# Kernel tuning notes

Measured on AMD Instinct MI355X. Metric: run time of the kernel, lower is better.

Reference implementation:

```python
import jax, jax.numpy as jnp
import numpy as np

DIM = 1024
HEADS = 16
DIM_HEAD = 64
INNER = HEADS * DIM_HEAD
SCALE = DIM_HEAD ** -0.5
LN_EPS = 1e-5
MASK_VALUE = -np.finfo(np.float32).max


def setup_inputs() -> dict:
    key = jax.random.key(0)
    ks = jax.random.split(key, 3)
    x = jax.random.normal(ks[0], (2, 2048, DIM), dtype=jnp.float32)
    w_qkv = jax.random.normal(ks[1], (DIM, 3 * INNER), dtype=jnp.float32) * (DIM ** -0.5)
    w_out = jax.random.normal(ks[2], (INNER, DIM), dtype=jnp.float32) * (INNER ** -0.5)
    ln_gamma = jnp.ones((DIM,), dtype=jnp.float32)
    ln_beta = jnp.zeros((DIM,), dtype=jnp.float32)
    return {"x": x, "ln_gamma": ln_gamma, "ln_beta": ln_beta, "w_qkv": w_qkv, "w_out": w_out}


def reference(x, ln_gamma, ln_beta, w_qkv, w_out):
    b, n, _ = x.shape
    # LayerNorm
    mu = jnp.mean(x, axis=-1, keepdims=True)
    var = jnp.mean(jnp.square(x - mu), axis=-1, keepdims=True)
    xn = (x - mu) * jax.lax.rsqrt(var + LN_EPS) * ln_gamma + ln_beta
    # QKV projection, split into heads: b n (h d) -> b h n d
    qkv = xn @ w_qkv  # [b, n, 3*inner]
    q, k, v = jnp.split(qkv, 3, axis=-1)
    def to_heads(t):
        return t.reshape(b, n, HEADS, DIM_HEAD).transpose(0, 2, 1, 3)
    q, k, v = to_heads(q), to_heads(k), to_heads(v)
    # scaled scores with diagonal excluded
    dots = jnp.einsum('bhnd,bhmd->bhnm', q, k) * SCALE
    eye = jnp.eye(n, dtype=bool)
    dots = jnp.where(eye, MASK_VALUE, dots)
    attn = jax.nn.softmax(dots, axis=-1)
    out = jnp.einsum('bhnm,bhmd->bhnd', attn, v)
    out = out.transpose(0, 2, 1, 3).reshape(b, n, INNER)
    return out @ w_out
```

## Files before the change

kernel.cpp:

```cpp
#include <hip/hip_runtime.h>


#define DIMM   1024
#define NSEQ   2048
#define BATCH  2
#define HEADS  16
#define DHEAD  64
#define QKVN   3072
#define MROWS  4096

typedef float          f32x4  __attribute__((ext_vector_type(4)));
typedef __bf16         bf16x8 __attribute__((ext_vector_type(8)));
typedef __bf16         bf16x4 __attribute__((ext_vector_type(4)));
typedef unsigned short u16x8  __attribute__((ext_vector_type(8)));
typedef unsigned short u16x4  __attribute__((ext_vector_type(4)));

#define QSCALE (0.125f * 1.4426950408889634f)

#if __has_builtin(__builtin_amdgcn_exp2f)
#define EXP2(x) __builtin_amdgcn_exp2f(x)
#else
#define EXP2(x) exp2f(x)
#endif

__device__ __forceinline__ unsigned short f2bf(float f) {
  unsigned u = __builtin_bit_cast(unsigned, f);
  u += 0x7FFFu + ((u >> 16) & 1u);
  return (unsigned short)(u >> 16);
}
__device__ __forceinline__ bf16x8 as_bf(u16x8 v) { return __builtin_bit_cast(bf16x8, v); }

__device__ __forceinline__ u16x4 cvt4(f32x4 v) {
  bf16x4 b;
  b[0] = (__bf16)v[0]; b[1] = (__bf16)v[1]; b[2] = (__bf16)v[2]; b[3] = (__bf16)v[3];
  return __builtin_bit_cast(u16x4, b);
}

__device__ __forceinline__ void gl_lds16(const unsigned short* g, unsigned short* l) {
  __builtin_amdgcn_global_load_lds(
      (const __attribute__((address_space(1))) unsigned*)g,
      (__attribute__((address_space(3))) unsigned*)l, 16, 0, 0);
}

__device__ __forceinline__ bf16x8 lds_frag(const unsigned short* base, int row, int chunk) {
  return as_bf(*(const u16x8*)&base[row * 64 + ((chunk ^ (row & 7)) << 3)]);
}

__device__ __forceinline__ bf16x8 lds_frag128(const unsigned short* base, int row, int chunk) {
  return as_bf(*(const u16x8*)&base[row * 128 + ((chunk ^ (row & 15)) << 3)]);
}

__device__ __forceinline__ void transpose_tile(
    const float* __restrict__ src, unsigned short* __restrict__ dst,
    int R, int C, int bx, int by, int tid) {
  __shared__ float t[32][33];
  const int rb = by * 32, cb = bx * 32;
  const int r0 = tid >> 5;
  const int c  = tid & 31;
#pragma unroll
  for (int i = 0; i < 4; ++i)
    t[r0 + i * 8][c] = src[(rb + r0 + i * 8) * C + cb + c];
  __syncthreads();
#pragma unroll
  for (int i = 0; i < 4; ++i)
    dst[(cb + r0 + i * 8) * R + rb + c] = f2bf(t[c][r0 + i * 8]);
}

__global__ __launch_bounds__(256) void prep_kernel(
    const float* __restrict__ x, const float* __restrict__ g,
    const float* __restrict__ be, const float* __restrict__ w_qkv,
    const float* __restrict__ w_out, unsigned short* __restrict__ xn,
    unsigned short* __restrict__ wqkvT, unsigned short* __restrict__ woutT) {
  const int bid = blockIdx.x, tid = threadIdx.x;
  if (bid < MROWS) {
    const int row = bid;
    const int wave = tid >> 6, lane = tid & 63;
    const float4 v = *(const float4*)&x[row * DIMM + tid * 4];
    float s  = v.x + v.y + v.z + v.w;
    float s2 = v.x * v.x + v.y * v.y + v.z * v.z + v.w * v.w;
#pragma unroll
    for (int o = 32; o >= 1; o >>= 1) { s += __shfl_xor(s, o); s2 += __shfl_xor(s2, o); }
    __shared__ float ps[4], ps2[4];
    if (lane == 0) { ps[wave] = s; ps2[wave] = s2; }
    __syncthreads();
    s  = ps[0] + ps[1] + ps[2] + ps[3];
    s2 = ps2[0] + ps2[1] + ps2[2] + ps2[3];
    const float mu  = s * (1.0f / DIMM);
    const float var = s2 * (1.0f / DIMM) - mu * mu;
    const float rs  = rsqrtf(var + 1e-5f);
    const float4 gg = *(const float4*)&g[tid * 4];
    const float4 bb = *(const float4*)&be[tid * 4];
    u16x4 o;
    o[0] = f2bf((v.x - mu) * rs * gg.x + bb.x);
    o[1] = f2bf((v.y - mu) * rs * gg.y + bb.y);
    o[2] = f2bf((v.z - mu) * rs * gg.z + bb.z);
    o[3] = f2bf((v.w - mu) * rs * gg.w + bb.w);
    *(u16x4*)&xn[row * DIMM + tid * 4] = o;
  } else {
    const int t = bid - MROWS;
    const int bx = t & 127, by = t >> 7;
    if (bx < QKVN / 32) transpose_tile(w_qkv, wqkvT, DIMM, QKVN, bx, by, tid);
    else                transpose_tile(w_out, woutT, DIMM, DIMM, bx - QKVN / 32, by, tid);
  }
}

__global__ __launch_bounds__(256, 3) void gemm_qkv_kernel(
    const unsigned short* __restrict__ A, const unsigned short* __restrict__ Bt,
    unsigned short* __restrict__ qb, unsigned short* __restrict__ kb,
    unsigned short* __restrict__ vtb) {
  __shared__ __attribute__((aligned(16))) unsigned short As[128 * 64];
  __shared__ __attribute__((aligned(16))) unsigned short Bs[128 * 64];
  const int tid = threadIdx.x;
  const int bm = blockIdx.y, bn = blockIdx.x;
  const int lane = tid & 63, wave = tid >> 6;
  const int l15 = lane & 15, quad = lane >> 4;
  const int wm = wave >> 1, wn = wave & 1;
  const int lrow = lane >> 3;
  const int gcol = ((lane & 7) ^ lrow) << 3;
  const unsigned short* Ab = A  + (bm * 128 + wave * 32 + lrow) * DIMM + gcol;
  const unsigned short* Bb = Bt + (bn * 128 + wave * 32 + lrow) * DIMM + gcol;
  const bool swap = (bn < 16);
  f32x4 acc[4][4] = {};

  for (int k0 = 0; k0 < DIMM; k0 += 64) {
#pragma unroll
    for (int j = 0; j < 4; ++j) {
      gl_lds16(Ab + j * 8 * DIMM + k0, &As[(wave * 32 + j * 8) * 64]);
      gl_lds16(Bb + j * 8 * DIMM + k0, &Bs[(wave * 32 + j * 8) * 64]);
    }
    __syncthreads();
#pragma unroll
    for (int kk = 0; kk < 2; ++kk) {
      bf16x8 af[4], bfr[4];
#pragma unroll
      for (int mi = 0; mi < 4; ++mi) af[mi]  = lds_frag(As, wm * 64 + mi * 16 + l15, kk * 4 + quad);
#pragma unroll
      for (int ni = 0; ni < 4; ++ni) bfr[ni] = lds_frag(Bs, wn * 64 + ni * 16 + l15, kk * 4 + quad);
      if (swap) {
#pragma unroll
        for (int mi = 0; mi < 4; ++mi)
#pragma unroll
          for (int ni = 0; ni < 4; ++ni)
            acc[mi][ni] = __builtin_amdgcn_mfma_f32_16x16x32_bf16(bfr[ni], af[mi], acc[mi][ni], 0, 0, 0);
      } else {
#pragma unroll
        for (int mi = 0; mi < 4; ++mi)
#pragma unroll
          for (int ni = 0; ni < 4; ++ni)
            acc[mi][ni] = __builtin_amdgcn_mfma_f32_16x16x32_bf16(af[mi], bfr[ni], acc[mi][ni], 0, 0, 0);
      }
    }
    __syncthreads();
  }

  if (swap) {
    const int colbase = bn * 128 + wn * 64;
    const int which = colbase >> 10;
    unsigned short* dst = which ? kb : qb;
    const float sc = which ? 1.0f : QSCALE;
#pragma unroll
    for (int mi = 0; mi < 4; ++mi) {
      const int m = bm * 128 + wm * 64 + mi * 16 + l15;
      const int bh0 = (m >> 11) * HEADS;
      const int n = m & 2047;
#pragma unroll
      for (int ni = 0; ni < 4; ++ni) {
        const int wc = (colbase & 1023) + ni * 16 + quad * 4;
        const int h = wc >> 6, dd = wc & 63;
        f32x4 v = acc[mi][ni] * sc;
        *(u16x4*)&dst[((bh0 + h) * NSEQ + n) * DHEAD + dd] = cvt4(v);
      }
    }
  } else {
    const int colbase = bn * 128 + wn * 64 - 2048;
#pragma unroll
    for (int mi = 0; mi < 4; ++mi) {
      const int m0 = bm * 128 + wm * 64 + mi * 16 + quad * 4;
      const int bh0 = (m0 >> 11) * HEADS;
      const int n0 = m0 & 2047;
#pragma unroll
      for (int ni = 0; ni < 4; ++ni) {
        const int vcol = colbase + ni * 16 + l15;
        const int h = vcol >> 6, dd = vcol & 63;
        *(u16x4*)&vtb[((bh0 + h) * DHEAD + dd) * NSEQ + n0] = cvt4(acc[mi][ni]);
      }
    }
  }
}

__global__ __launch_bounds__(256, 2) void attn_kernel(
    const unsigned short* __restrict__ qb, const unsigned short* __restrict__ kb,
    const unsigned short* __restrict__ vtb, unsigned short* __restrict__ attn_out) {
  __shared__ __attribute__((aligned(16))) unsigned short Ks[2][64 * 64];
  __shared__ __attribute__((aligned(16))) unsigned short Vts[2][64 * 64];
  __shared__ __attribute__((aligned(16))) unsigned short Ps[4][2][16][72];
  const int tid = threadIdx.x, wave = tid >> 6, lane = tid & 63;
  const int l15 = lane & 15, quad = lane >> 4;
  const int bh = blockIdx.x, qt = blockIdx.y;
  const int b = bh >> 4, h = bh & 15;
  const int qbase = qt * 128 + wave * 32;

  bf16x8 aq[2][2];
#pragma unroll
  for (int sub = 0; sub < 2; ++sub) {
    const unsigned short* qrow = qb + (bh * NSEQ + qbase + sub * 16 + l15) * DHEAD;
    aq[sub][0] = as_bf(*(const u16x8*)(qrow + quad * 8));
    aq[sub][1] = as_bf(*(const u16x8*)(qrow + 32 + quad * 8));
  }

  float lsum[2] = {0.f, 0.f};
  f32x4 occ[2][4] = {};

  const int lrow = lane >> 3;
  const int gcol = ((lane & 7) ^ lrow) << 3;
  const unsigned short* Kb = kb  + (bh * NSEQ + wave * 16 + lrow) * DHEAD + gcol;
  const unsigned short* Vb = vtb + (bh * DHEAD + wave * 16 + lrow) * NSEQ + gcol;

  gl_lds16(Kb,             &Ks[0][(wave * 16) * 64]);
  gl_lds16(Kb + 8 * DHEAD, &Ks[0][(wave * 16 + 8) * 64]);
  gl_lds16(Vb,             &Vts[0][(wave * 16) * 64]);
  gl_lds16(Vb + 8 * NSEQ,  &Vts[0][(wave * 16 + 8) * 64]);

  const int diag_it = qt * 2 + (wave >> 1);

  for (int it = 0; it < NSEQ / 64; ++it) {
    const int cur = it & 1;
    __syncthreads();
    if (it < NSEQ / 64 - 1) {
      const unsigned short* Kn = Kb + (it + 1) * 64 * DHEAD;
      const unsigned short* Vn = Vb + (it + 1) * 64;
      gl_lds16(Kn,             &Ks[cur ^ 1][(wave * 16) * 64]);
      gl_lds16(Kn + 8 * DHEAD, &Ks[cur ^ 1][(wave * 16 + 8) * 64]);
      gl_lds16(Vn,             &Vts[cur ^ 1][(wave * 16) * 64]);
      gl_lds16(Vn + 8 * NSEQ,  &Vts[cur ^ 1][(wave * 16 + 8) * 64]);
    }
    bf16x8 ak[2][4], av[2][4];
#pragma unroll
    for (int kk = 0; kk < 2; ++kk)
#pragma unroll
      for (int ct = 0; ct < 4; ++ct) {
        ak[kk][ct] = lds_frag(&Ks[cur][0],  ct * 16 + l15, kk * 4 + quad);
        av[kk][ct] = lds_frag(&Vts[cur][0], ct * 16 + l15, kk * 4 + quad);
      }

    f32x4 scc[2][4];
#pragma unroll
    for (int sub = 0; sub < 2; ++sub)
#pragma unroll
      for (int ct = 0; ct < 4; ++ct) scc[sub][ct] = (f32x4){-32.f, -32.f, -32.f, -32.f};
    __builtin_amdgcn_s_setprio(1);
#pragma unroll
    for (int sub = 0; sub < 2; ++sub)
#pragma unroll
      for (int kk = 0; kk < 2; ++kk)
#pragma unroll
        for (int ct = 0; ct < 4; ++ct)
          scc[sub][ct] = __builtin_amdgcn_mfma_f32_16x16x32_bf16(ak[kk][ct], aq[sub][kk], scc[sub][ct], 0, 0, 0);
    __builtin_amdgcn_s_setprio(0);

#pragma unroll
    for (int sub = 0; sub < 2; ++sub)
#pragma unroll
      for (int ct = 0; ct < 4; ++ct)
#pragma unroll
        for (int r = 0; r < 4; ++r) scc[sub][ct][r] = EXP2(scc[sub][ct][r]);

    if (it == diag_it) {
#pragma unroll
      for (int sub = 0; sub < 2; ++sub) {
        const int kvo_want = (wave & 1) * 32 + sub * 16 + l15;
#pragma unroll
        for (int ct = 0; ct < 4; ++ct)
#pragma unroll
          for (int r = 0; r < 4; ++r)
            if (ct * 16 + quad * 4 + r == kvo_want) scc[sub][ct][r] = 0.f;
      }
    }

#pragma unroll
    for (int sub = 0; sub < 2; ++sub) {
      f32x4 ps4 = (scc[sub][0] + scc[sub][1]) + (scc[sub][2] + scc[sub][3]);
      lsum[sub] += (ps4[0] + ps4[1]) + (ps4[2] + ps4[3]);
    }

#pragma unroll
    for (int sub = 0; sub < 2; ++sub)
#pragma unroll
      for (int ct = 0; ct < 4; ++ct)
        *(u16x4*)&Ps[wave][sub][l15][ct * 16 + quad * 4] = cvt4(scc[sub][ct]);

    bf16x8 bp[2][2];
#pragma unroll
    for (int sub = 0; sub < 2; ++sub)
#pragma unroll
      for (int kk = 0; kk < 2; ++kk)
        bp[sub][kk] = as_bf(*(const u16x8*)&Ps[wave][sub][l15][kk * 32 + quad * 8]);

    __builtin_amdgcn_s_setprio(1);
#pragma unroll
    for (int sub = 0; sub < 2; ++sub)
#pragma unroll
      for (int kk = 0; kk < 2; ++kk)
#pragma unroll
        for (int ct = 0; ct < 4; ++ct)
          occ[sub][ct] = __builtin_amdgcn_mfma_f32_16x16x32_bf16(av[kk][ct], bp[sub][kk], occ[sub][ct], 0, 0, 0);
    __builtin_amdgcn_s_setprio(0);
  }
#pragma unroll
  for (int sub = 0; sub < 2; ++sub) {
    float l = lsum[sub];
    l += __shfl_xor(l, 16);
    l += __shfl_xor(l, 32);
    const float rl = __builtin_amdgcn_rcpf(l);
    const int qg = qbase + sub * 16 + l15;
#pragma unroll
    for (int ct = 0; ct < 4; ++ct) {
      f32x4 ov = occ[sub][ct] * rl;
      *(u16x4*)&attn_out[(b * NSEQ + qg) * DIMM + h * DHEAD + ct * 16 + quad * 4] = cvt4(ov);
    }
  }
}

__global__ __launch_bounds__(256, 2) void gemm_out_kernel(
    const unsigned short* __restrict__ A,
    const unsigned short* __restrict__ Bt,
    float* __restrict__ out) {
  __shared__ __attribute__((aligned(16))) unsigned short As[64 * 128];
  __shared__ __attribute__((aligned(16))) unsigned short Bs[128 * 128];
  const int tid = threadIdx.x;
  const int bm = blockIdx.y, bn = blockIdx.x;
  const int lane = tid & 63, wave = tid >> 6;
  const int l15 = lane & 15, quad = lane >> 4;
  const int wm = wave >> 1, wn = wave & 1;
  const int rl4 = lane >> 4;
  const int cp  = lane & 15;
  const int cx  = cp ^ rl4;
  const int Arow0 = bm * 64 + wave * 16 + rl4;
  const int Brow0 = bn * 128 + wave * 32 + rl4;
  f32x4 acc[2][4] = {};

  for (int it = 0; it < 8; ++it) {
    const int k0 = it * 128;
#pragma unroll
    for (int j = 0; j < 4; ++j)
      gl_lds16(A + (Arow0 + j * 4) * DIMM + k0 + ((cx ^ (j << 2)) << 3),
               &As[(wave * 16 + j * 4) * 128]);
#pragma unroll
    for (int j = 0; j < 8; ++j)
      gl_lds16(Bt + (Brow0 + j * 4) * DIMM + k0 + ((cx ^ ((j & 3) << 2)) << 3),
               &Bs[(wave * 32 + j * 4) * 128]);
    __syncthreads();
#pragma unroll
    for (int kk = 0; kk < 4; ++kk) {
      bf16x8 af[2], bfr[4];
#pragma unroll
      for (int mi = 0; mi < 2; ++mi) af[mi]  = lds_frag128(As, wm * 32 + mi * 16 + l15, kk * 4 + quad);
#pragma unroll
      for (int ni = 0; ni < 4; ++ni) bfr[ni] = lds_frag128(Bs, wn * 64 + ni * 16 + l15, kk * 4 + quad);
#pragma unroll
      for (int mi = 0; mi < 2; ++mi)
#pragma unroll
        for (int ni = 0; ni < 4; ++ni)
          acc[mi][ni] = __builtin_amdgcn_mfma_f32_16x16x32_bf16(bfr[ni], af[mi], acc[mi][ni], 0, 0, 0);
    }
    __syncthreads();
  }
#pragma unroll
  for (int mi = 0; mi < 2; ++mi) {
    const int m = bm * 64 + wm * 32 + mi * 16 + l15;
#pragma unroll
    for (int ni = 0; ni < 4; ++ni) {
      const int col = bn * 128 + wn * 64 + ni * 16 + quad * 4;
      *(f32x4*)&out[m * DIMM + col] = acc[mi][ni];
    }
  }
}

extern "C" void kernel_launch(void* const* d_in, const int* in_sizes, int n_in,
                              void* d_out, int out_size, void* d_ws, size_t ws_size,
                              hipStream_t stream) {
  const float* x     = (const float*)d_in[0];
  const float* gamma = (const float*)d_in[1];
  const float* beta  = (const float*)d_in[2];
  const float* w_qkv = (const float*)d_in[3];
  const float* w_out = (const float*)d_in[4];
  float* out = (float*)d_out;

  char* ws = (char*)d_ws;
  unsigned short* xn    = (unsigned short*)(ws);
  unsigned short* wqkvT = (unsigned short*)(ws + 8388608);
  unsigned short* woutT = (unsigned short*)(ws + 14680064);
  unsigned short* qbuf  = (unsigned short*)(ws + 16777216);
  unsigned short* kbuf  = (unsigned short*)(ws + 25165824);
  unsigned short* vtbuf = (unsigned short*)(ws + 33554432);
  unsigned short* attnb = (unsigned short*)(ws + 41943040);

  prep_kernel<<<MROWS + (QKVN + DIMM) / 32 * (DIMM / 32), 256, 0, stream>>>(
      x, gamma, beta, w_qkv, w_out, xn, wqkvT, woutT);
  gemm_qkv_kernel<<<dim3(24, MROWS / 128), 256, 0, stream>>>(xn, wqkvT, qbuf, kbuf, vtbuf);
  attn_kernel<<<dim3(BATCH * HEADS, NSEQ / 128), 256, 0, stream>>>(qbuf, kbuf, vtbuf, attnb);
  gemm_out_kernel<<<dim3(DIMM / 128, MROWS / 64), 256, 0, stream>>>(attnb, woutT, out);
}
```

Measured before the change: 180.4 us.

## Split attention KV tile across wave pairs with 64-query waves and LDS reduction

```diff
diff --git a/kernel.cpp b/kernel.cpp
--- a/kernel.cpp
+++ b/kernel.cpp
@@ -191,37 +191,39 @@
 __global__ __launch_bounds__(256, 2) void attn_kernel(
     const unsigned short* __restrict__ qb, const unsigned short* __restrict__ kb,
     const unsigned short* __restrict__ vtb, unsigned short* __restrict__ attn_out) {
-  __shared__ __attribute__((aligned(16))) unsigned short Ks[2][64 * 64];
-  __shared__ __attribute__((aligned(16))) unsigned short Vts[2][64 * 64];
-  __shared__ __attribute__((aligned(16))) unsigned short Ps[4][2][16][72];
+  __shared__ __attribute__((aligned(16))) unsigned short KVs[4][64 * 64];
+  __shared__ __attribute__((aligned(16))) unsigned short Ps[4][64][40];
+  __shared__ float Lred[2][4][16];
   const int tid = threadIdx.x, wave = tid >> 6, lane = tid & 63;
   const int l15 = lane & 15, quad = lane >> 4;
   const int bh = blockIdx.x, qt = blockIdx.y;
   const int b = bh >> 4, h = bh & 15;
-  const int qbase = qt * 128 + wave * 32;
-
-  bf16x8 aq[2][2];
-#pragma unroll
-  for (int sub = 0; sub < 2; ++sub) {
-    const unsigned short* qrow = qb + (bh * NSEQ + qbase + sub * 16 + l15) * DHEAD;
-    aq[sub][0] = as_bf(*(const u16x8*)(qrow + quad * 8));
-    aq[sub][1] = as_bf(*(const u16x8*)(qrow + 32 + quad * 8));
-  }
-
-  float lsum[2] = {0.f, 0.f};
-  f32x4 occ[2][4] = {};
+  const int jq = wave & 1;
+  const int ikv = wave >> 1;
+  const int qbase = qt * 128 + jq * 64;
+
+  bf16x8 aq[4][2];
+#pragma unroll
+  for (int nt = 0; nt < 4; ++nt) {
+    const unsigned short* qrow = qb + (bh * NSEQ + qbase + nt * 16 + l15) * DHEAD;
+    aq[nt][0] = as_bf(*(const u16x8*)(qrow + quad * 8));
+    aq[nt][1] = as_bf(*(const u16x8*)(qrow + 32 + quad * 8));
+  }
+
+  float lsum[4] = {0.f, 0.f, 0.f, 0.f};
+  f32x4 occ[4][4] = {};
 
   const int lrow = lane >> 3;
   const int gcol = ((lane & 7) ^ lrow) << 3;
   const unsigned short* Kb = kb  + (bh * NSEQ + wave * 16 + lrow) * DHEAD + gcol;
   const unsigned short* Vb = vtb + (bh * DHEAD + wave * 16 + lrow) * NSEQ + gcol;
 
-  gl_lds16(Kb,             &Ks[0][(wave * 16) * 64]);
-  gl_lds16(Kb + 8 * DHEAD, &Ks[0][(wave * 16 + 8) * 64]);
-  gl_lds16(Vb,             &Vts[0][(wave * 16) * 64]);
-  gl_lds16(Vb + 8 * NSEQ,  &Vts[0][(wave * 16 + 8) * 64]);
-
-  const int diag_it = qt * 2 + (wave >> 1);
+  gl_lds16(Kb,             &KVs[0][(wave * 16) * 64]);
+  gl_lds16(Kb + 8 * DHEAD, &KVs[0][(wave * 16 + 8) * 64]);
+  gl_lds16(Vb,             &KVs[2][(wave * 16) * 64]);
+  gl_lds16(Vb + 8 * NSEQ,  &KVs[2][(wave * 16 + 8) * 64]);
+
+  const int diag_it = qt * 2 + jq;
 
   for (int it = 0; it < NSEQ / 64; ++it) {
     const int cur = it & 1;
@@ -229,94 +231,118 @@
     if (it < NSEQ / 64 - 1) {
       const unsigned short* Kn = Kb + (it + 1) * 64 * DHEAD;
       const unsigned short* Vn = Vb + (it + 1) * 64;
-      gl_lds16(Kn,             &Ks[cur ^ 1][(wave * 16) * 64]);
-      gl_lds16(Kn + 8 * DHEAD, &Ks[cur ^ 1][(wave * 16 + 8) * 64]);
-      gl_lds16(Vn,             &Vts[cur ^ 1][(wave * 16) * 64]);
-      gl_lds16(Vn + 8 * NSEQ,  &Vts[cur ^ 1][(wave * 16 + 8) * 64]);
-    }
-    bf16x8 ak[2][4], av[2][4];
+      gl_lds16(Kn,             &KVs[cur ^ 1][(wave * 16) * 64]);
+      gl_lds16(Kn + 8 * DHEAD, &KVs[cur ^ 1][(wave * 16 + 8) * 64]);
+      gl_lds16(Vn,             &KVs[2 + (cur ^ 1)][(wave * 16) * 64]);
+      gl_lds16(Vn + 8 * NSEQ,  &KVs[2 + (cur ^ 1)][(wave * 16 + 8) * 64]);
+    }
+    bf16x8 ak[2][2];
 #pragma unroll
     for (int kk = 0; kk < 2; ++kk)
 #pragma unroll
+      for (int mt = 0; mt < 2; ++mt)
+        ak[kk][mt] = lds_frag(&KVs[cur][0], ikv * 32 + mt * 16 + l15, kk * 4 + quad);
+    bf16x8 av[4];
+#pragma unroll
+    for (int ct = 0; ct < 4; ++ct)
+      av[ct] = lds_frag(&KVs[2 + cur][0], ct * 16 + l15, ikv * 4 + quad);
+
+    f32x4 scc[2][4];
+#pragma unroll
+    for (int mt = 0; mt < 2; ++mt)
+#pragma unroll
+      for (int nt = 0; nt < 4; ++nt) scc[mt][nt] = (f32x4){-32.f, -32.f, -32.f, -32.f};
+    __builtin_amdgcn_s_setprio(1);
+#pragma unroll
+    for (int kk = 0; kk < 2; ++kk)
+#pragma unroll
+      for (int mt = 0; mt < 2; ++mt)
+#pragma unroll
+        for (int nt = 0; nt < 4; ++nt)
+          scc[mt][nt] = __builtin_amdgcn_mfma_f32_16x16x32_bf16(ak[kk][mt], aq[nt][kk], scc[mt][nt], 0, 0, 0);
+    __builtin_amdgcn_s_setprio(0);
+
+#pragma unroll
+    for (int mt = 0; mt < 2; ++mt)
+#pragma unroll
+      for (int nt = 0; nt < 4; ++nt)
+#pragma unroll
+        for (int r = 0; r < 4; ++r) scc[mt][nt][r] = EXP2(scc[mt][nt][r]);
+
+    if (it == diag_it) {
+#pragma unroll
+      for (int nt = 0; nt < 4; ++nt) {
+        if ((nt >> 1) == ikv) {
+          const int mtm = nt & 1;
+#pragma unroll
+          for (int r = 0; r < 4; ++r)
+            if (quad * 4 + r == l15) scc[mtm][nt][r] = 0.f;
+        }
+      }
+    }
+
+#pragma unroll
+    for (int nt = 0; nt < 4; ++nt) {
+      f32x4 t = scc[0][nt] + scc[1][nt];
+      lsum[nt] += (t[0] + t[1]) + (t[2] + t[3]);
+    }
+
+#pragma unroll
+    for (int mt = 0; mt < 2; ++mt)
+#pragma unroll
+      for (int nt = 0; nt < 4; ++nt)
+        *(u16x4*)&Ps[wave][nt * 16 + l15][mt * 16 + quad * 4] = cvt4(scc[mt][nt]);
+
+    bf16x8 bp[4];
+#pragma unroll
+    for (int nt = 0; nt < 4; ++nt)
+      bp[nt] = as_bf(*(const u16x8*)&Ps[wave][nt * 16 + l15][quad * 8]);
+
+    __builtin_amdgcn_s_setprio(1);
+#pragma unroll
+    for (int ct = 0; ct < 4; ++ct)
+#pragma unroll
+      for (int nt = 0; nt < 4; ++nt)
+        occ[ct][nt] = __builtin_amdgcn_mfma_f32_16x16x32_bf16(av[ct], bp[nt], occ[ct][nt], 0, 0, 0);
+    __builtin_amdgcn_s_setprio(0);
+  }
+
+#pragma unroll
+  for (int nt = 0; nt < 4; ++nt) {
+    lsum[nt] += __shfl_xor(lsum[nt], 16);
+    lsum[nt] += __shfl_xor(lsum[nt], 32);
+  }
+
+  __syncthreads();
+  float* Ored = (float*)&KVs[0][0];
+  if (ikv == 1) {
+#pragma unroll
+    for (int ct = 0; ct < 4; ++ct)
+#pragma unroll
+      for (int nt = 0; nt < 4; ++nt)
+        *(f32x4*)&Ored[((jq * 16 + ct * 4 + nt) * 64 + lane) * 4] = occ[ct][nt];
+    if (quad == 0) {
+#pragma unroll
+      for (int nt = 0; nt < 4; ++nt) Lred[jq][nt][l15] = lsum[nt];
+    }
+  }
+  __syncthreads();
+  if (ikv == 0) {
+#pragma unroll
+    for (int ct = 0; ct < 4; ++ct)
+#pragma unroll
+      for (int nt = 0; nt < 4; ++nt)
+        occ[ct][nt] += *(const f32x4*)&Ored[((jq * 16 + ct * 4 + nt) * 64 + lane) * 4];
+#pragma unroll
+    for (int nt = 0; nt < 4; ++nt) {
+      const float l = lsum[nt] + Lred[jq][nt][l15];
+      const float rl = __builtin_amdgcn_rcpf(l);
+      const int qg = qbase + nt * 16 + l15;
+#pragma unroll
       for (int ct = 0; ct < 4; ++ct) {
-        ak[kk][ct] = lds_frag(&Ks[cur][0],  ct * 16 + l15, kk * 4 + quad);
-        av[kk][ct] = lds_frag(&Vts[cur][0], ct * 16 + l15, kk * 4 + quad);
+        f32x4 ov = occ[ct][nt] * rl;
+        *(u16x4*)&attn_out[(b * NSEQ + qg) * DIMM + h * DHEAD + ct * 16 + quad * 4] = cvt4(ov);
       }
-
-    f32x4 scc[2][4];
-#pragma unroll
-    for (int sub = 0; sub < 2; ++sub)
-#pragma unroll
-      for (int ct = 0; ct < 4; ++ct) scc[sub][ct] = (f32x4){-32.f, -32.f, -32.f, -32.f};
-    __builtin_amdgcn_s_setprio(1);
-#pragma unroll
-    for (int sub = 0; sub < 2; ++sub)
-#pragma unroll
-      for (int kk = 0; kk < 2; ++kk)
-#pragma unroll
-        for (int ct = 0; ct < 4; ++ct)
-          scc[sub][ct] = __builtin_amdgcn_mfma_f32_16x16x32_bf16(ak[kk][ct], aq[sub][kk], scc[sub][ct], 0, 0, 0);
-    __builtin_amdgcn_s_setprio(0);
-
-#pragma unroll
-    for (int sub = 0; sub < 2; ++sub)
-#pragma unroll
-      for (int ct = 0; ct < 4; ++ct)
-#pragma unroll
-        for (int r = 0; r < 4; ++r) scc[sub][ct][r] = EXP2(scc[sub][ct][r]);
-
-    if (it == diag_it) {
-#pragma unroll
-      for (int sub = 0; sub < 2; ++sub) {
-        const int kvo_want = (wave & 1) * 32 + sub * 16 + l15;
-#pragma unroll
-        for (int ct = 0; ct < 4; ++ct)
-#pragma unroll
-          for (int r = 0; r < 4; ++r)
-            if (ct * 16 + quad * 4 + r == kvo_want) scc[sub][ct][r] = 0.f;
-      }
-    }
-
-#pragma unroll
-    for (int sub = 0; sub < 2; ++sub) {
-      f32x4 ps4 = (scc[sub][0] + scc[sub][1]) + (scc[sub][2] + scc[sub][3]);
-      lsum[sub] += (ps4[0] + ps4[1]) + (ps4[2] + ps4[3]);
-    }
-
-#pragma unroll
-    for (int sub = 0; sub < 2; ++sub)
-#pragma unroll
-      for (int ct = 0; ct < 4; ++ct)
-        *(u16x4*)&Ps[wave][sub][l15][ct * 16 + quad * 4] = cvt4(scc[sub][ct]);
-
-    bf16x8 bp[2][2];
-#pragma unroll
-    for (int sub = 0; sub < 2; ++sub)
-#pragma unroll
-      for (int kk = 0; kk < 2; ++kk)
-        bp[sub][kk] = as_bf(*(const u16x8*)&Ps[wave][sub][l15][kk * 32 + quad * 8]);
-
-    __builtin_amdgcn_s_setprio(1);
-#pragma unroll
-    for (int sub = 0; sub < 2; ++sub)
-#pragma unroll
-      for (int kk = 0; kk < 2; ++kk)
-#pragma unroll
-        for (int ct = 0; ct < 4; ++ct)
-          occ[sub][ct] = __builtin_amdgcn_mfma_f32_16x16x32_bf16(av[kk][ct], bp[sub][kk], occ[sub][ct], 0, 0, 0);
-    __builtin_amdgcn_s_setprio(0);
-  }
-#pragma unroll
-  for (int sub = 0; sub < 2; ++sub) {
-    float l = lsum[sub];
-    l += __shfl_xor(l, 16);
-    l += __shfl_xor(l, 32);
-    const float rl = __builtin_amdgcn_rcpf(l);
-    const int qg = qbase + sub * 16 + l15;
-#pragma unroll
-    for (int ct = 0; ct < 4; ++ct) {
-      f32x4 ov = occ[sub][ct] * rl;
-      *(u16x4*)&attn_out[(b * NSEQ + qg) * DIMM + h * DHEAD + ct * 16 + quad * 4] = cvt4(ov);
     }
   }
 }
```

Measured after the change: 187.9 us. 1.04x slower.
